# Performance work log

Measured on AMD Instinct MI355X. Metric: run time of the kernel, lower is better.

Reference implementation:

```python
import jax, jax.numpy as jnp
import numpy as np
import math

B, S, D, H = 2, 2048, 1024, 16
DK = D // H


def setup_inputs() -> dict:
    key = jax.random.key(0)
    ks = jax.random.split(key, 14)
    inp = {
        "query": jax.random.normal(ks[0], (B, S, D), dtype=jnp.float32),
        "key": jax.random.normal(ks[1], (B, S, D), dtype=jnp.float32),
        "value": jax.random.normal(ks[2], (B, S, D), dtype=jnp.float32),
        "group_prob": jax.random.uniform(ks[3], (B, S, S), dtype=jnp.float32),
        "mask": jax.random.randint(ks[4], (B, S), 0, 2, dtype=jnp.int32),
    }
    scale = 0.02
    inp["Wq"] = jax.random.normal(ks[5], (D, D), dtype=jnp.float32) * scale
    inp["bq"] = jnp.zeros((D,), dtype=jnp.float32)
    inp["Wk"] = jax.random.normal(ks[6], (D, D), dtype=jnp.float32) * scale
    inp["bk"] = jnp.zeros((D,), dtype=jnp.float32)
    inp["Wv"] = jax.random.normal(ks[7], (D, D), dtype=jnp.float32) * scale
    inp["bv"] = jnp.zeros((D,), dtype=jnp.float32)
    inp["Wo"] = jax.random.normal(ks[8], (D, D), dtype=jnp.float32) * scale
    inp["bo"] = jnp.zeros((D,), dtype=jnp.float32)
    return inp


def reference(query, key, value, group_prob, mask, Wq, bq, Wk, bk, Wv, bv, Wo, bo):
    b, s, d = query.shape
    # project and split heads: [B,S,D] -> [B,H,S,DK]
    def proj(x, W, bias):
        return (x @ W.T + bias).reshape(b, s, H, DK).transpose(0, 2, 1, 3)

    q = proj(query, Wq, bq)
    k = proj(key, Wk, bk)
    v = proj(value, Wv, bv)

    scores = jnp.einsum("bhqd,bhkd->bhqk", q, k) / math.sqrt(DK)  # [B,H,S,S]

    # combined mask: padding-row mask OR diagonal (always attend to self)
    eye = jnp.eye(s, dtype=jnp.int32)
    combined = mask[:, None, None, :] | eye[None, None, :, :]  # [B,1,S,S]
    scores = jnp.where(combined == 0, jnp.float32(-1e9), scores)

    p_attn = jax.nn.softmax(scores, axis=-1)
    p_attn = p_attn * group_prob[:, None, :, :]  # post-softmax group scaling

    x = jnp.einsum("bhqk,bhkd->bhqd", p_attn, v)  # [B,H,S,DK]
    x = x.transpose(0, 2, 1, 3).reshape(b, s, d)
    return x @ Wo.T + bo
```

## Files before the change

kernel.cpp:

```cpp
#include <hip/hip_runtime.h>
#include <hip/hip_bf16.h>
#include <stdint.h>

typedef __bf16 bf16x8 __attribute__((ext_vector_type(8)));
typedef float f32x4 __attribute__((ext_vector_type(4)));

__device__ __forceinline__ void gld16(const void* g, void* l) {
  __builtin_amdgcn_global_load_lds(
      (__attribute__((address_space(1))) void*)(uintptr_t)(g),
      (__attribute__((address_space(3))) void*)(l), 16, 0, 0);
}

struct CastArgs {
  const float* src[7];
  __bf16* dst[7];
  int n[7];
};

__global__ __launch_bounds__(256) void cast_bf16_kernel(CastArgs a) {
  const int t = blockIdx.y;
  const int i = (blockIdx.x * 256 + threadIdx.x) * 8;
  if (i >= a.n[t]) return;
  const float4* s = (const float4*)(a.src[t] + i);
  float4 v0 = s[0], v1 = s[1];
  bf16x8 o;
  o[0] = (__bf16)v0.x; o[1] = (__bf16)v0.y; o[2] = (__bf16)v0.z; o[3] = (__bf16)v0.w;
  o[4] = (__bf16)v1.x; o[5] = (__bf16)v1.y; o[6] = (__bf16)v1.z; o[7] = (__bf16)v1.w;
  *(bf16x8*)(a.dst[t] + i) = o;
}

__global__ __launch_bounds__(256) void cast_gp_kernel(const float* __restrict__ src,
                                                      __bf16* __restrict__ dst) {
  const int i = (blockIdx.x * 256 + threadIdx.x) * 8;
  const float4* s = (const float4*)(src + i);
  float4 v0 = s[0], v1 = s[1];
  bf16x8 o;
  o[0] = (__bf16)v0.x; o[1] = (__bf16)v0.y; o[2] = (__bf16)v0.z; o[3] = (__bf16)v0.w;
  o[4] = (__bf16)v1.x; o[5] = (__bf16)v1.y; o[6] = (__bf16)v1.z; o[7] = (__bf16)v1.w;
  *(bf16x8*)(dst + i) = o;
}

template <int MODE>
__global__ __launch_bounds__(256) void gemm_bt(const __bf16* __restrict__ A,
                                               const __bf16* __restrict__ B,
                                               const float* __restrict__ bias,
                                               void* __restrict__ outp, float scale) {
  __shared__ __align__(16) __bf16 As[128 * 32];
  __shared__ __align__(16) __bf16 Bs[128 * 32];
  const int tid = threadIdx.x;
  const int m0 = blockIdx.y * 128;
  const int n0 = blockIdx.x * 128;
  const int lane = tid & 63, wid = tid >> 6;
  const int wm = (wid & 1) * 64, wn = (wid >> 1) * 64;
  const int l16 = lane & 15, quad = lane >> 4;

  const int sc = (tid & 3) ^ ((tid >> 2) & 3);
  const __bf16* ga = A + (size_t)(m0 + (tid >> 2)) * 1024 + sc * 8;
  const __bf16* gb = B + (size_t)(n0 + (tid >> 2)) * 1024 + sc * 8;
  char* lA = (char*)As + tid * 16;
  char* lB = (char*)Bs + tid * 16;
  const int a_off = (wm + l16) * 64 + ((quad ^ (l16 & 3)) * 16);
  const int b_off = (wn + l16) * 64 + ((quad ^ (l16 & 3)) * 16);

  f32x4 acc[4][4] = {};

  for (int k0 = 0; k0 < 1024; k0 += 32) {
    __syncthreads();
    gld16(ga + k0, lA);
    gld16(ga + k0 + 64 * 1024, lA + 4096);
    gld16(gb + k0, lB);
    gld16(gb + k0 + 64 * 1024, lB + 4096);
    __syncthreads();
    bf16x8 af[4], bfr[4];
#pragma unroll
    for (int mi = 0; mi < 4; ++mi)
      af[mi] = *(const bf16x8*)((const char*)As + a_off + mi * 1024);
#pragma unroll
    for (int ni = 0; ni < 4; ++ni)
      bfr[ni] = *(const bf16x8*)((const char*)Bs + b_off + ni * 1024);
#pragma unroll
    for (int mi = 0; mi < 4; ++mi)
#pragma unroll
      for (int ni = 0; ni < 4; ++ni)
        acc[mi][ni] = __builtin_amdgcn_mfma_f32_16x16x32_bf16(af[mi], bfr[ni],
                                                              acc[mi][ni], 0, 0, 0);
  }

  if (MODE == 2) {
    float* out = (float*)outp;
#pragma unroll
    for (int ni = 0; ni < 4; ++ni) {
      const int col = n0 + wn + ni * 16 + l16;
      const float bb = bias[col];
#pragma unroll
      for (int mi = 0; mi < 4; ++mi)
#pragma unroll
        for (int r = 0; r < 4; ++r) {
          const int row = m0 + wm + mi * 16 + quad * 4 + r;
          out[(size_t)row * 1024 + col] = (acc[mi][ni][r] + bb) * scale;
        }
    }
  } else if (MODE == 0) {
    __bf16* out = (__bf16*)outp;
#pragma unroll
    for (int ni = 0; ni < 4; ++ni) {
      const int col = n0 + wn + ni * 16 + l16;
      const int h = col >> 6, dk = col & 63;
      const float bb = bias[col];
#pragma unroll
      for (int mi = 0; mi < 4; ++mi)
#pragma unroll
        for (int r = 0; r < 4; ++r) {
          const int row = m0 + wm + mi * 16 + quad * 4 + r;
          const int b = row >> 11, s = row & 2047;
          out[((size_t)(b * 16 + h) * 2048 + s) * 64 + dk] =
              (__bf16)((acc[mi][ni][r] + bb) * scale);
        }
    }
  } else {
    __bf16* out = (__bf16*)outp;
#pragma unroll
    for (int mi = 0; mi < 4; ++mi)
#pragma unroll
      for (int r = 0; r < 4; ++r) {
        const int rowm = m0 + wm + mi * 16 + quad * 4 + r;
        const int h = rowm >> 6, dk = rowm & 63;
        const float bb = bias[rowm];
#pragma unroll
        for (int ni = 0; ni < 4; ++ni) {
          const int coln = n0 + wn + ni * 16 + l16;
          const int b = coln >> 11, s = coln & 2047;
          out[((size_t)(b * 16 + h) * 64 + dk) * 2048 + s] =
              (__bf16)((acc[mi][ni][r] + bb) * scale);
        }
      }
  }
}

__global__ __launch_bounds__(256) void attn_kernel(
    const __bf16* __restrict__ Qh, const __bf16* __restrict__ Kh,
    const __bf16* __restrict__ Vt, const __bf16* __restrict__ gp16,
    const int* __restrict__ maskp, __bf16* __restrict__ xb) {
  __shared__ __align__(16) __bf16 Qs[64 * 64];
  __shared__ __align__(16) __bf16 Ks[64 * 64];
  __shared__ __align__(16) __bf16 Vs[64 * 64];
  __shared__ __align__(16) __bf16 Ps[4][16 * 64];

  const int tid = threadIdx.x;
  const int qt = blockIdx.x, bh = blockIdx.y;
  const int b = bh >> 4, h = bh & 15;
  const int q0 = qt * 64;
  const int lane = tid & 63, wid = tid >> 6, l16 = lane & 15, quad = lane >> 4;
  const size_t head_off = (size_t)bh * (2048 * 64);

  const int srow = tid >> 3;
  const int sc8 = (tid & 7) ^ (srow & 7);
  const int fxor = (l16 & 7);

  {
    const __bf16* gq = Qh + head_off + (size_t)(q0 + srow) * 64 + sc8 * 8;
    gld16(gq, (char*)Qs + tid * 16);
    gld16(gq + 32 * 64, (char*)Qs + 4096 + tid * 16);
  }
  __syncthreads();
  bf16x8 aq[2];
  aq[0] = *(const bf16x8*)((const char*)Qs + (wid * 16 + l16) * 128 +
                           ((quad ^ fxor) * 16));
  aq[1] = *(const bf16x8*)((const char*)Qs + (wid * 16 + l16) * 128 +
                           (((4 + quad) ^ fxor) * 16));

  f32x4 o[4] = {};
  float lp[4] = {0.f, 0.f, 0.f, 0.f};
  int irow[4];
#pragma unroll
  for (int r = 0; r < 4; ++r) irow[r] = q0 + wid * 16 + quad * 4 + r;

  const __bf16* gk0 = Kh + head_off + (size_t)srow * 64 + sc8 * 8;
  const __bf16* gv0 = Vt + head_off + (size_t)srow * 2048 + sc8 * 8;
  const int* mrow = maskp + b * 2048;
  const __bf16* gpb = gp16 + (size_t)b * 2048 * 2048;

  for (int kt = 0; kt < 32; ++kt) {
    __syncthreads();
    gld16(gk0 + kt * 4096, (char*)Ks + tid * 16);
    gld16(gk0 + kt * 4096 + 2048, (char*)Ks + 4096 + tid * 16);
    gld16(gv0 + kt * 64, (char*)Vs + tid * 16);
    gld16(gv0 + kt * 64 + 32 * 2048, (char*)Vs + 4096 + tid * 16);

    const int jbase = kt * 64;
    int mj[4];
#pragma unroll
    for (int ni = 0; ni < 4; ++ni) mj[ni] = mrow[jbase + ni * 16 + l16];
    float gf[4][4];
#pragma unroll
    for (int r = 0; r < 4; ++r) {
      const __bf16* gpr = gpb + (size_t)irow[r] * 2048 + jbase + l16;
#pragma unroll
      for (int ni = 0; ni < 4; ++ni) gf[ni][r] = (float)gpr[ni * 16];
    }
    __syncthreads();

    f32x4 sc[4] = {};
#pragma unroll
    for (int kh = 0; kh < 2; ++kh)
#pragma unroll
      for (int ni = 0; ni < 4; ++ni) {
        bf16x8 bk = *(const bf16x8*)((const char*)Ks + (ni * 16 + l16) * 128 +
                                     (((kh * 4 + quad) ^ fxor) * 16));
        sc[ni] = __builtin_amdgcn_mfma_f32_16x16x32_bf16(aq[kh], bk, sc[ni], 0, 0, 0);
      }

    float pv[4][4];
    if (kt != qt) {
#pragma unroll
      for (int ni = 0; ni < 4; ++ni)
#pragma unroll
        for (int r = 0; r < 4; ++r) {
          const float e = __expf(sc[ni][r]);
          const float p = (mj[ni] != 0) ? e : 0.f;
          lp[r] += p;
          pv[ni][r] = p * gf[ni][r];
        }
    } else {
#pragma unroll
      for (int ni = 0; ni < 4; ++ni)
#pragma unroll
        for (int r = 0; r < 4; ++r) {
          const float e = __expf(sc[ni][r]);
          const bool diag = (ni == wid) && (l16 == quad * 4 + r);
          const float p = (mj[ni] != 0 || diag) ? e : 0.f;
          lp[r] += p;
          pv[ni][r] = p * gf[ni][r];
        }
    }

#pragma unroll
    for (int ni = 0; ni < 4; ++ni)
#pragma unroll
      for (int r = 0; r < 4; ++r) {
        const int prow = quad * 4 + r;
        const int pchunk = (ni * 2 + (l16 >> 3)) ^ (prow & 7);
        *(__bf16*)((char*)&Ps[wid][0] + prow * 128 + pchunk * 16 + (l16 & 7) * 2) =
            (__bf16)pv[ni][r];
      }
    asm volatile("s_waitcnt lgkmcnt(0)" ::: "memory");

#pragma unroll
    for (int kh = 0; kh < 2; ++kh) {
      bf16x8 ap = *(const bf16x8*)((const char*)&Ps[wid][0] + l16 * 128 +
                                   (((kh * 4 + quad) ^ fxor) * 16));
#pragma unroll
      for (int ni = 0; ni < 4; ++ni) {
        bf16x8 bv = *(const bf16x8*)((const char*)Vs + (ni * 16 + l16) * 128 +
                                     (((kh * 4 + quad) ^ fxor) * 16));
        o[ni] = __builtin_amdgcn_mfma_f32_16x16x32_bf16(ap, bv, o[ni], 0, 0, 0);
      }
    }
  }

#pragma unroll
  for (int r = 0; r < 4; ++r) {
    lp[r] += __shfl_xor(lp[r], 1);
    lp[r] += __shfl_xor(lp[r], 2);
    lp[r] += __shfl_xor(lp[r], 4);
    lp[r] += __shfl_xor(lp[r], 8);
    lp[r] = 1.f / lp[r];
  }
#pragma unroll
  for (int ni = 0; ni < 4; ++ni) {
    const int dk = ni * 16 + l16;
#pragma unroll
    for (int r = 0; r < 4; ++r) {
      const float val = o[ni][r] * lp[r];
      xb[((size_t)(b * 2048 + irow[r])) * 1024 + h * 64 + dk] = (__bf16)val;
    }
  }
}

extern "C" void kernel_launch(void* const* d_in, const int* in_sizes, int n_in,
                              void* d_out, int out_size, void* d_ws, size_t ws_size,
                              hipStream_t stream) {
  const float* query = (const float*)d_in[0];
  const float* key_  = (const float*)d_in[1];
  const float* value = (const float*)d_in[2];
  const float* gprob = (const float*)d_in[3];
  const int*   maskp = (const int*)d_in[4];
  const float* Wq = (const float*)d_in[5];
  const float* bq = (const float*)d_in[6];
  const float* Wk = (const float*)d_in[7];
  const float* bk = (const float*)d_in[8];
  const float* Wv = (const float*)d_in[9];
  const float* bv = (const float*)d_in[10];
  const float* Wo = (const float*)d_in[11];
  const float* bo = (const float*)d_in[12];

  char* ws = (char*)d_ws;
  const size_t MB = 1 << 20;
  __bf16* qb  = (__bf16*)(ws + 0 * MB);
  __bf16* kb  = (__bf16*)(ws + 8 * MB);
  __bf16* vb  = (__bf16*)(ws + 16 * MB);
  __bf16* Wqb = (__bf16*)(ws + 24 * MB);
  __bf16* Wkb = (__bf16*)(ws + 26 * MB);
  __bf16* Wvb = (__bf16*)(ws + 28 * MB);
  __bf16* Wob = (__bf16*)(ws + 30 * MB);
  __bf16* Qh  = (__bf16*)(ws + 32 * MB);
  __bf16* Kh  = (__bf16*)(ws + 40 * MB);
  __bf16* Vt  = (__bf16*)(ws + 48 * MB);
  __bf16* xb  = (__bf16*)(ws + 56 * MB);
  __bf16* gp16 = (__bf16*)(ws + 0 * MB);

  CastArgs ca;
  ca.src[0] = query; ca.dst[0] = qb;  ca.n[0] = 4194304;
  ca.src[1] = key_;  ca.dst[1] = kb;  ca.n[1] = 4194304;
  ca.src[2] = value; ca.dst[2] = vb;  ca.n[2] = 4194304;
  ca.src[3] = Wq;    ca.dst[3] = Wqb; ca.n[3] = 1048576;
  ca.src[4] = Wk;    ca.dst[4] = Wkb; ca.n[4] = 1048576;
  ca.src[5] = Wv;    ca.dst[5] = Wvb; ca.n[5] = 1048576;
  ca.src[6] = Wo;    ca.dst[6] = Wob; ca.n[6] = 1048576;

  cast_bf16_kernel<<<dim3(2048, 7), 256, 0, stream>>>(ca);
  gemm_bt<0><<<dim3(8, 32), 256, 0, stream>>>(qb, Wqb, bq, Qh, 0.125f);
  gemm_bt<0><<<dim3(8, 32), 256, 0, stream>>>(kb, Wkb, bk, Kh, 1.0f);
  gemm_bt<1><<<dim3(32, 8), 256, 0, stream>>>(Wvb, vb, bv, Vt, 1.0f);
  cast_gp_kernel<<<dim3(4096), 256, 0, stream>>>(gprob, gp16);
  attn_kernel<<<dim3(32, 32), 256, 0, stream>>>(Qh, Kh, Vt, gp16, maskp, xb);
  gemm_bt<2><<<dim3(8, 32), 256, 0, stream>>>(xb, Wob, bo, (float*)d_out, 1.0f);
}
```

Before: 353.4 us.

## Batch QKV GEMMs in one launch, vectorize group-prob loads, bitpack mask

The three Q/K/V projection GEMMs are merged into a single launch with a z-dimension selecting operands, which removes two launches and lets the three GEMMs share the GPU together. In the attention kernel, the key mask is turned into per-tile 64-bit ballot bitmasks in shared memory, replacing per-tile int loads. Group probabilities are now loaded as two 16-byte vectors per lane in the row layout of the P operand, instead of 16 scalar bf16 loads, and are multiplied into P after it is read back from LDS. The row sum still uses the unscaled probabilities, so the math is unchanged, but there is an extra bf16 rounding step in the P*g product.

Result: faster. 333.5 us (-5.6%).

```diff
diff --git a/kernel.cpp b/kernel.cpp
--- a/kernel.cpp
+++ b/kernel.cpp
@@ -40,11 +40,102 @@
   *(bf16x8*)(dst + i) = o;
 }
 
-template <int MODE>
-__global__ __launch_bounds__(256) void gemm_bt(const __bf16* __restrict__ A,
-                                               const __bf16* __restrict__ B,
-                                               const float* __restrict__ bias,
-                                               void* __restrict__ outp, float scale) {
+struct QkvArgs {
+  const __bf16* A[3];
+  const __bf16* B[3];
+  const float* bias[3];
+  __bf16* out[3];
+};
+
+__global__ __launch_bounds__(256) void qkv_gemm(QkvArgs args) {
+  __shared__ __align__(16) __bf16 As[128 * 32];
+  __shared__ __align__(16) __bf16 Bs[128 * 32];
+  const int tid = threadIdx.x;
+  const int z = blockIdx.y;
+  const int bx = blockIdx.x;
+  const int m0 = (z < 2 ? (bx >> 3) : (bx & 7)) * 128;
+  const int n0 = (z < 2 ? (bx & 7) : (bx >> 3)) * 128;
+  const __bf16* A = args.A[z];
+  const __bf16* B = args.B[z];
+  const float* bias = args.bias[z];
+  __bf16* out = args.out[z];
+  const float scale = (z == 0) ? 0.125f : 1.0f;
+
+  const int lane = tid & 63, wid = tid >> 6;
+  const int wm = (wid & 1) * 64, wn = (wid >> 1) * 64;
+  const int l16 = lane & 15, quad = lane >> 4;
+
+  const int sc = (tid & 3) ^ ((tid >> 2) & 3);
+  const __bf16* ga = A + (size_t)(m0 + (tid >> 2)) * 1024 + sc * 8;
+  const __bf16* gb = B + (size_t)(n0 + (tid >> 2)) * 1024 + sc * 8;
+  char* lA = (char*)As + tid * 16;
+  char* lB = (char*)Bs + tid * 16;
+  const int a_off = (wm + l16) * 64 + ((quad ^ (l16 & 3)) * 16);
+  const int b_off = (wn + l16) * 64 + ((quad ^ (l16 & 3)) * 16);
+
+  f32x4 acc[4][4] = {};
+
+  for (int k0 = 0; k0 < 1024; k0 += 32) {
+    __syncthreads();
+    gld16(ga + k0, lA);
+    gld16(ga + k0 + 64 * 1024, lA + 4096);
+    gld16(gb + k0, lB);
+    gld16(gb + k0 + 64 * 1024, lB + 4096);
+    __syncthreads();
+    bf16x8 af[4], bfr[4];
+#pragma unroll
+    for (int mi = 0; mi < 4; ++mi)
+      af[mi] = *(const bf16x8*)((const char*)As + a_off + mi * 1024);
+#pragma unroll
+    for (int ni = 0; ni < 4; ++ni)
+      bfr[ni] = *(const bf16x8*)((const char*)Bs + b_off + ni * 1024);
+#pragma unroll
+    for (int mi = 0; mi < 4; ++mi)
+#pragma unroll
+      for (int ni = 0; ni < 4; ++ni)
+        acc[mi][ni] = __builtin_amdgcn_mfma_f32_16x16x32_bf16(af[mi], bfr[ni],
+                                                              acc[mi][ni], 0, 0, 0);
+  }
+
+  if (z < 2) {
+#pragma unroll
+    for (int ni = 0; ni < 4; ++ni) {
+      const int col = n0 + wn + ni * 16 + l16;
+      const int h = col >> 6, dk = col & 63;
+      const float bb = bias[col];
+#pragma unroll
+      for (int mi = 0; mi < 4; ++mi)
+#pragma unroll
+        for (int r = 0; r < 4; ++r) {
+          const int row = m0 + wm + mi * 16 + quad * 4 + r;
+          const int b = row >> 11, s = row & 2047;
+          out[((size_t)(b * 16 + h) * 2048 + s) * 64 + dk] =
+              (__bf16)((acc[mi][ni][r] + bb) * scale);
+        }
+    }
+  } else {
+#pragma unroll
+    for (int mi = 0; mi < 4; ++mi)
+#pragma unroll
+      for (int r = 0; r < 4; ++r) {
+        const int rowm = m0 + wm + mi * 16 + quad * 4 + r;
+        const int h = rowm >> 6, dk = rowm & 63;
+        const float bb = bias[rowm];
+#pragma unroll
+        for (int ni = 0; ni < 4; ++ni) {
+          const int coln = n0 + wn + ni * 16 + l16;
+          const int b = coln >> 11, s = coln & 2047;
+          out[((size_t)(b * 16 + h) * 64 + dk) * 2048 + s] =
+              (__bf16)(acc[mi][ni][r] + bb);
+        }
+      }
+  }
+}
+
+__global__ __launch_bounds__(256) void gemm_out(const __bf16* __restrict__ A,
+                                                const __bf16* __restrict__ B,
+                                                const float* __restrict__ bias,
+                                                float* __restrict__ out) {
   __shared__ __align__(16) __bf16 As[128 * 32];
   __shared__ __align__(16) __bf16 Bs[128 * 32];
   const int tid = threadIdx.x;
@@ -86,53 +177,16 @@
                                                               acc[mi][ni], 0, 0, 0);
   }
 
-  if (MODE == 2) {
-    float* out = (float*)outp;
-#pragma unroll
-    for (int ni = 0; ni < 4; ++ni) {
-      const int col = n0 + wn + ni * 16 + l16;
-      const float bb = bias[col];
-#pragma unroll
-      for (int mi = 0; mi < 4; ++mi)
-#pragma unroll
-        for (int r = 0; r < 4; ++r) {
-          const int row = m0 + wm + mi * 16 + quad * 4 + r;
-          out[(size_t)row * 1024 + col] = (acc[mi][ni][r] + bb) * scale;
-        }
-    }
-  } else if (MODE == 0) {
-    __bf16* out = (__bf16*)outp;
-#pragma unroll
-    for (int ni = 0; ni < 4; ++ni) {
-      const int col = n0 + wn + ni * 16 + l16;
-      const int h = col >> 6, dk = col & 63;
-      const float bb = bias[col];
-#pragma unroll
-      for (int mi = 0; mi < 4; ++mi)
-#pragma unroll
-        for (int r = 0; r < 4; ++r) {
-          const int row = m0 + wm + mi * 16 + quad * 4 + r;
-          const int b = row >> 11, s = row & 2047;
-          out[((size_t)(b * 16 + h) * 2048 + s) * 64 + dk] =
-              (__bf16)((acc[mi][ni][r] + bb) * scale);
-        }
-    }
-  } else {
-    __bf16* out = (__bf16*)outp;
+#pragma unroll
+  for (int ni = 0; ni < 4; ++ni) {
+    const int col = n0 + wn + ni * 16 + l16;
+    const float bb = bias[col];
 #pragma unroll
     for (int mi = 0; mi < 4; ++mi)
 #pragma unroll
       for (int r = 0; r < 4; ++r) {
-        const int rowm = m0 + wm + mi * 16 + quad * 4 + r;
-        const int h = rowm >> 6, dk = rowm & 63;
-        const float bb = bias[rowm];
-#pragma unroll
-        for (int ni = 0; ni < 4; ++ni) {
-          const int coln = n0 + wn + ni * 16 + l16;
-          const int b = coln >> 11, s = coln & 2047;
-          out[((size_t)(b * 16 + h) * 64 + dk) * 2048 + s] =
-              (__bf16)((acc[mi][ni][r] + bb) * scale);
-        }
+        const int row = m0 + wm + mi * 16 + quad * 4 + r;
+        out[(size_t)row * 1024 + col] = acc[mi][ni][r] + bb;
       }
   }
 }
@@ -145,6 +199,7 @@
   __shared__ __align__(16) __bf16 Ks[64 * 64];
   __shared__ __align__(16) __bf16 Vs[64 * 64];
   __shared__ __align__(16) __bf16 Ps[4][16 * 64];
+  __shared__ unsigned long long mbits[32];
 
   const int tid = threadIdx.x;
   const int qt = blockIdx.x, bh = blockIdx.y;
@@ -162,6 +217,16 @@
     gld16(gq, (char*)Qs + tid * 16);
     gld16(gq + 32 * 64, (char*)Qs + 4096 + tid * 16);
   }
+  {
+    const int* mr = maskp + b * 2048;
+#pragma unroll
+    for (int t = 0; t < 8; ++t) {
+      const int kt2 = wid * 8 + t;
+      const int mv = mr[kt2 * 64 + lane];
+      const unsigned long long bal = __ballot(mv != 0);
+      if (lane == 0) mbits[kt2] = bal;
+    }
+  }
   __syncthreads();
   bf16x8 aq[2];
   aq[0] = *(const bf16x8*)((const char*)Qs + (wid * 16 + l16) * 128 +
@@ -177,8 +242,8 @@
 
   const __bf16* gk0 = Kh + head_off + (size_t)srow * 64 + sc8 * 8;
   const __bf16* gv0 = Vt + head_off + (size_t)srow * 2048 + sc8 * 8;
-  const int* mrow = maskp + b * 2048;
-  const __bf16* gpb = gp16 + (size_t)b * 2048 * 2048;
+  const __bf16* gpl = gp16 + (size_t)b * 2048 * 2048 +
+                      (size_t)(q0 + wid * 16 + l16) * 2048 + quad * 8;
 
   for (int kt = 0; kt < 32; ++kt) {
     __syncthreads();
@@ -187,17 +252,13 @@
     gld16(gv0 + kt * 64, (char*)Vs + tid * 16);
     gld16(gv0 + kt * 64 + 32 * 2048, (char*)Vs + 4096 + tid * 16);
 
-    const int jbase = kt * 64;
-    int mj[4];
-#pragma unroll
-    for (int ni = 0; ni < 4; ++ni) mj[ni] = mrow[jbase + ni * 16 + l16];
-    float gf[4][4];
-#pragma unroll
-    for (int r = 0; r < 4; ++r) {
-      const __bf16* gpr = gpb + (size_t)irow[r] * 2048 + jbase + l16;
-#pragma unroll
-      for (int ni = 0; ni < 4; ++ni) gf[ni][r] = (float)gpr[ni * 16];
-    }
+    bf16x8 g8_0 = *(const bf16x8*)(gpl + kt * 64);
+    bf16x8 g8_1 = *(const bf16x8*)(gpl + kt * 64 + 32);
+
+    const unsigned long long sh = mbits[kt] >> l16;
+    const uint32_t shlo = (uint32_t)sh, shhi = (uint32_t)(sh >> 32);
+    const bool mk[4] = {(shlo & 1) != 0, (shlo & 0x10000u) != 0,
+                        (shhi & 1) != 0, (shhi & 0x10000u) != 0};
     __syncthreads();
 
     f32x4 sc[4] = {};
@@ -210,16 +271,16 @@
         sc[ni] = __builtin_amdgcn_mfma_f32_16x16x32_bf16(aq[kh], bk, sc[ni], 0, 0, 0);
       }
 
-    float pv[4][4];
+    float pw[4][4];
     if (kt != qt) {
 #pragma unroll
       for (int ni = 0; ni < 4; ++ni)
 #pragma unroll
         for (int r = 0; r < 4; ++r) {
           const float e = __expf(sc[ni][r]);
-          const float p = (mj[ni] != 0) ? e : 0.f;
+          const float p = mk[ni] ? e : 0.f;
           lp[r] += p;
-          pv[ni][r] = p * gf[ni][r];
+          pw[ni][r] = p;
         }
     } else {
 #pragma unroll
@@ -228,9 +289,9 @@
         for (int r = 0; r < 4; ++r) {
           const float e = __expf(sc[ni][r]);
           const bool diag = (ni == wid) && (l16 == quad * 4 + r);
-          const float p = (mj[ni] != 0 || diag) ? e : 0.f;
+          const float p = (mk[ni] || diag) ? e : 0.f;
           lp[r] += p;
-          pv[ni][r] = p * gf[ni][r];
+          pw[ni][r] = p;
         }
     }
 
@@ -241,7 +302,7 @@
         const int prow = quad * 4 + r;
         const int pchunk = (ni * 2 + (l16 >> 3)) ^ (prow & 7);
         *(__bf16*)((char*)&Ps[wid][0] + prow * 128 + pchunk * 16 + (l16 & 7) * 2) =
-            (__bf16)pv[ni][r];
+            (__bf16)pw[ni][r];
       }
     asm volatile("s_waitcnt lgkmcnt(0)" ::: "memory");
 
@@ -249,11 +310,16 @@
     for (int kh = 0; kh < 2; ++kh) {
       bf16x8 ap = *(const bf16x8*)((const char*)&Ps[wid][0] + l16 * 128 +
                                    (((kh * 4 + quad) ^ fxor) * 16));
+      const bf16x8 g8 = kh ? g8_1 : g8_0;
+      bf16x8 apg;
+#pragma unroll
+      for (int j = 0; j < 8; ++j)
+        apg[j] = (__bf16)((float)ap[j] * (float)g8[j]);
 #pragma unroll
       for (int ni = 0; ni < 4; ++ni) {
         bf16x8 bv = *(const bf16x8*)((const char*)Vs + (ni * 16 + l16) * 128 +
                                      (((kh * 4 + quad) ^ fxor) * 16));
-        o[ni] = __builtin_amdgcn_mfma_f32_16x16x32_bf16(ap, bv, o[ni], 0, 0, 0);
+        o[ni] = __builtin_amdgcn_mfma_f32_16x16x32_bf16(apg, bv, o[ni], 0, 0, 0);
       }
     }
   }
@@ -317,12 +383,15 @@
   ca.src[4] = Wk;    ca.dst[4] = Wkb; ca.n[4] = 1048576;
   ca.src[5] = Wv;    ca.dst[5] = Wvb; ca.n[5] = 1048576;
   ca.src[6] = Wo;    ca.dst[6] = Wob; ca.n[6] = 1048576;
-
   cast_bf16_kernel<<<dim3(2048, 7), 256, 0, stream>>>(ca);
-  gemm_bt<0><<<dim3(8, 32), 256, 0, stream>>>(qb, Wqb, bq, Qh, 0.125f);
-  gemm_bt<0><<<dim3(8, 32), 256, 0, stream>>>(kb, Wkb, bk, Kh, 1.0f);
-  gemm_bt<1><<<dim3(32, 8), 256, 0, stream>>>(Wvb, vb, bv, Vt, 1.0f);
+
+  QkvArgs qa;
+  qa.A[0] = qb;  qa.B[0] = Wqb; qa.bias[0] = bq; qa.out[0] = Qh;
+  qa.A[1] = kb;  qa.B[1] = Wkb; qa.bias[1] = bk; qa.out[1] = Kh;
+  qa.A[2] = Wvb; qa.B[2] = vb;  qa.bias[2] = bv; qa.out[2] = Vt;
+  qkv_gemm<<<dim3(256, 3), 256, 0, stream>>>(qa);
+
   cast_gp_kernel<<<dim3(4096), 256, 0, stream>>>(gprob, gp16);
   attn_kernel<<<dim3(32, 32), 256, 0, stream>>>(Qh, Kh, Vt, gp16, maskp, xb);
-  gemm_bt<2><<<dim3(8, 32), 256, 0, stream>>>(xb, Wob, bo, (float*)d_out, 1.0f);
-}
+  gemm_out<<<dim3(8, 32), 256, 0, stream>>>(xb, Wob, bo, (float*)d_out);
+}
```
